# Performance work log

Hardware: AMD Instinct MI355X
Metric: run time of the kernel (lower is better)

Reference implementation:

```python
import jax, jax.numpy as jnp
import numpy as np

# AWQ packing: nibble for unpacked column j (within a packed int32 of 8 values)
# lives at bit offset 4 * AWQ_ORDER[j]  (the 'reverse AWQ order').
AWQ_ORDER = (0, 4, 1, 5, 2, 6, 3, 7)
GROUP_SIZE = 128


def _unpack_int4(packed):
    """[R, C] int32 -> [R, 8*C] int32 of 4-bit values in AWQ order."""
    shifts = jnp.array(AWQ_ORDER, dtype=jnp.int32) * 4  # [8]
    nib = jnp.right_shift(packed[:, :, None], shifts) & 0xF  # [R, C, 8]
    return nib.reshape(packed.shape[0], -1)


def setup_inputs() -> dict:
    key = jax.random.key(0)
    k1, k2, k3, k4 = jax.random.split(key, 4)
    M, K, N = 1024, 4096, 11008
    G = K // GROUP_SIZE  # 32
    x = jax.random.normal(k1, (M, K), dtype=jnp.float32)
    imin = jnp.iinfo(jnp.int32).min
    imax = jnp.iinfo(jnp.int32).max
    qweight = jax.random.randint(k2, (K, N // 8), imin, imax, dtype=jnp.int32)
    qzeros = jax.random.randint(k3, (G, N // 8), imin, imax, dtype=jnp.int32)
    scales = jax.random.uniform(k4, (G, N), dtype=jnp.float32, minval=0.001, maxval=0.01)
    return {"x": x, "qweight": qweight, "scales": scales, "qzeros": qzeros}


def reference(x, qweight, scales, qzeros):
    # Dequantize: W[k, n] = (w4[k, n] - z4[k//gs, n]) * scales[k//gs, n]
    K = qweight.shape[0]
    gs = K // qzeros.shape[0]  # group size
    w4 = _unpack_int4(qweight).astype(jnp.float32)   # [K, N]
    z4 = _unpack_int4(qzeros).astype(jnp.float32)    # [G, N]
    z = jnp.repeat(z4, gs, axis=0)                   # [K, N]
    s = jnp.repeat(scales, gs, axis=0)               # [K, N]
    W = (w4 - z) * s                                 # [K, N]
    # FP16_MATMUL_HEURISTIC path: dequantize then plain matmul
    return jnp.matmul(x, W)                          # [M, N]
```

## Files before the change

### kernel.cpp

```cpp
#include <hip/hip_runtime.h>
#include <stdint.h>

#define M_DIM 1024
#define K_DIM 4096
#define N_DIM 11008
#define NC_DIM 1376
#define G_DIM 32
#define GS 128

typedef __bf16 bf16x8 __attribute__((ext_vector_type(8)));
typedef float f32x4 __attribute__((ext_vector_type(4)));
typedef unsigned short ushort8 __attribute__((ext_vector_type(8)));

typedef __attribute__((address_space(1))) char as1_char;
typedef __attribute__((address_space(3))) char as3_char;
#define GLDS16(g, l) __builtin_amdgcn_global_load_lds((as1_char*)(g), (as3_char*)(l), 16, 0, 0)

static __device__ __forceinline__ int awq_shift(int j) {
  return ((j & 1) << 4) | ((j >> 1) << 2);
}

static __device__ __forceinline__ unsigned short f2bf(float f) {
  union { float f; uint32_t u; } c; c.f = f;
  uint32_t u = c.u;
  return (unsigned short)((u + 0x7FFFu + ((u >> 16) & 1u)) >> 16);
}

__global__ void k_cvt_x(const float* __restrict__ x, unsigned short* __restrict__ xb) {
  int i = blockIdx.x * blockDim.x + threadIdx.x;
  int base = i * 8;
  float4 v0 = *(const float4*)(x + base);
  float4 v1 = *(const float4*)(x + base + 4);
  ushort8 o;
  o[0] = f2bf(v0.x); o[1] = f2bf(v0.y); o[2] = f2bf(v0.z); o[3] = f2bf(v0.w);
  o[4] = f2bf(v1.x); o[5] = f2bf(v1.y); o[6] = f2bf(v1.z); o[7] = f2bf(v1.w);
  *(ushort8*)(xb + base) = o;
}

__global__ void k_dequant(const int* __restrict__ qw, const float* __restrict__ scales,
                          const int* __restrict__ qz, unsigned short* __restrict__ wt) {
  __shared__ int wlds[64][17];
  const int t = threadIdx.x;
  const int k0 = blockIdx.x * 64;
  const int nb = blockIdx.y;
  const int n_glob0 = nb * 128;
  const int c0 = n_glob0 >> 3;
  const int g = k0 >> 7;
#pragma unroll
  for (int p = 0; p < 4; ++p) {
    int idx = p * 256 + t;
    int k = idx >> 4, c = idx & 15;
    wlds[k][c] = qw[(size_t)(k0 + k) * NC_DIM + c0 + c];
  }
  __syncthreads();
#pragma unroll
  for (int p = 0; p < 4; ++p) {
    int u = p * 256 + t;
    int k8 = u & 7;
    int nl = u >> 3;
    int j = nl & 7;
    int c = nl >> 3;
    int shift = awq_shift(j);
    float s = scales[(size_t)g * N_DIM + n_glob0 + nl];
    int zw = qz[(size_t)g * NC_DIM + c0 + c];
    float zs = (float)((zw >> shift) & 0xF) * s;
    ushort8 o;
#pragma unroll
    for (int i = 0; i < 8; ++i) {
      int wv = wlds[k8 * 8 + i][c];
      int nib = (wv >> shift) & 0xF;
      o[i] = f2bf(fmaf((float)nib, s, -zs));
    }
    *(ushort8*)(wt + (size_t)(nb * 128 + nl) * K_DIM + k0 + k8 * 8) = o;
  }
}

#define BK 64
#define NT (K_DIM / BK)
#define REG_BYTES 16384

__device__ __forceinline__ void stage_half(const unsigned short* __restrict__ src, int row0, int T,
                                           unsigned char* lds_region, int w, int lane) {
  const int kb = (((lane & 7) ^ ((lane >> 3) & 7)) << 4);
  const int row = w * 16 + (lane >> 3);
  const unsigned short* g = src + (size_t)(row0 + row) * K_DIM + T * 64 + (kb >> 1);
  unsigned char* l = lds_region + w * 2048;
  GLDS16(g, l);
  GLDS16(g + (size_t)8 * K_DIM, l + 1024);
}

#define RD(base, off) (*(const bf16x8*)((const unsigned char*)(base) + (off)))
#define MFMA16(a, b, c) __builtin_amdgcn_mfma_f32_16x16x32_bf16((a), (b), (c), 0, 0, 0)

__launch_bounds__(512, 2)
__global__ void k_gemm8(const unsigned short* __restrict__ A,
                        const unsigned short* __restrict__ Bt,
                        float* __restrict__ C) {
  __shared__ __attribute__((aligned(16))) unsigned char LDS[131072];

  const int tid = threadIdx.x;
  const int lane = tid & 63;
  const int w = tid >> 6;
  const int wm = w >> 2;
  const int wn = w & 3;
  const int u = lane & 15;
  const int h = lane >> 4;
  const int xor16 = (lane & 7) << 4;
  const int kpos0 = (h * 16) ^ xor16;
  const int kpos1 = (64 + h * 16) ^ xor16;
  const int aoff = u * 128;

  const int orig = blockIdx.x;
  const int xcd = orig & 7, loc = orig >> 3;
  const int qq = 21, rr = 4;
  const int swz = (xcd < rr) ? xcd * (qq + 1) + loc : rr * (qq + 1) + (xcd - rr) * qq + loc;
  const int m0 = (swz & 3) * 256;
  const int nb0 = (swz >> 2) * 256;

  f32x4 acc[8][4] = {};

  stage_half(A,  m0,        0, LDS + 0 * REG_BYTES, w, lane);
  stage_half(A,  m0 + 128,  0, LDS + 1 * REG_BYTES, w, lane);
  stage_half(Bt, nb0,       0, LDS + 2 * REG_BYTES, w, lane);
  stage_half(Bt, nb0 + 128, 0, LDS + 3 * REG_BYTES, w, lane);
  stage_half(Bt, nb0,       1, LDS + 65536 + 2 * REG_BYTES, w, lane);
  stage_half(A,  m0,        1, LDS + 65536 + 0 * REG_BYTES, w, lane);
  asm volatile("s_waitcnt vmcnt(4)" ::: "memory");
  __builtin_amdgcn_s_barrier();

#pragma unroll 2
  for (int t = 0; t < NT; ++t) {
    const int cur = t & 1;
    unsigned char* bufc = LDS + cur * 65536;
    unsigned char* bufn = LDS + (cur ^ 1) * 65536;
    const unsigned char* rA = bufc + wm * REG_BYTES;
    const unsigned char* rB = bufc + (2 + (wn >> 1)) * REG_BYTES;
    const int bsub = (wn & 1) * 8192;

    bf16x8 aR[4][2], bLo[2][2], bHi[2][2];

#pragma unroll
    for (int mi = 0; mi < 4; ++mi) {
      aR[mi][0] = RD(rA, mi * 2048 + aoff + kpos0);
      aR[mi][1] = RD(rA, mi * 2048 + aoff + kpos1);
    }
#pragma unroll
    for (int nf = 0; nf < 2; ++nf) {
      bLo[nf][0] = RD(rB, bsub + nf * 2048 + aoff + kpos0);
      bLo[nf][1] = RD(rB, bsub + nf * 2048 + aoff + kpos1);
    }
    if (t + 1 < NT) stage_half(A, m0 + 128, t + 1, bufn + 1 * REG_BYTES, w, lane);
    __builtin_amdgcn_s_barrier();
    __builtin_amdgcn_s_setprio(1);
#pragma unroll
    for (int mi = 0; mi < 4; ++mi)
#pragma unroll
      for (int nf = 0; nf < 2; ++nf) {
        acc[mi][nf] = MFMA16(aR[mi][0], bLo[nf][0], acc[mi][nf]);
        acc[mi][nf] = MFMA16(aR[mi][1], bLo[nf][1], acc[mi][nf]);
      }
    __builtin_amdgcn_s_setprio(0);
    __builtin_amdgcn_s_barrier();

#pragma unroll
    for (int nf = 0; nf < 2; ++nf) {
      bHi[nf][0] = RD(rB, bsub + (nf + 2) * 2048 + aoff + kpos0);
      bHi[nf][1] = RD(rB, bsub + (nf + 2) * 2048 + aoff + kpos1);
    }
    if (t + 1 < NT) stage_half(Bt, nb0 + 128, t + 1, bufn + 3 * REG_BYTES, w, lane);
    __builtin_amdgcn_s_barrier();
    __builtin_amdgcn_s_setprio(1);
#pragma unroll
    for (int mi = 0; mi < 4; ++mi)
#pragma unroll
      for (int nf = 0; nf < 2; ++nf) {
        acc[mi][nf + 2] = MFMA16(aR[mi][0], bHi[nf][0], acc[mi][nf + 2]);
        acc[mi][nf + 2] = MFMA16(aR[mi][1], bHi[nf][1], acc[mi][nf + 2]);
      }
    __builtin_amdgcn_s_setprio(0);
    __builtin_amdgcn_s_barrier();

#pragma unroll
    for (int mi = 0; mi < 4; ++mi) {
      aR[mi][0] = RD(rA, (mi + 4) * 2048 + aoff + kpos0);
      aR[mi][1] = RD(rA, (mi + 4) * 2048 + aoff + kpos1);
    }
    if (t + 2 < NT) stage_half(Bt, nb0, t + 2, bufc + 2 * REG_BYTES, w, lane);
    __builtin_amdgcn_s_barrier();
    __builtin_amdgcn_s_setprio(1);
#pragma unroll
    for (int mi = 0; mi < 4; ++mi)
#pragma unroll
      for (int nf = 0; nf < 2; ++nf) {
        acc[mi + 4][nf + 2] = MFMA16(aR[mi][0], bHi[nf][0], acc[mi + 4][nf + 2]);
        acc[mi + 4][nf + 2] = MFMA16(aR[mi][1], bHi[nf][1], acc[mi + 4][nf + 2]);
      }
    __builtin_amdgcn_s_setprio(0);
    __builtin_amdgcn_s_barrier();

    if (t + 2 < NT) stage_half(A, m0, t + 2, bufc + 0 * REG_BYTES, w, lane);
    __builtin_amdgcn_s_barrier();
    __builtin_amdgcn_s_setprio(1);
#pragma unroll
    for (int mi = 0; mi < 4; ++mi)
#pragma unroll
      for (int nf = 0; nf < 2; ++nf) {
        acc[mi + 4][nf] = MFMA16(aR[mi][0], bLo[nf][0], acc[mi + 4][nf]);
        acc[mi + 4][nf] = MFMA16(aR[mi][1], bLo[nf][1], acc[mi + 4][nf]);
      }
    __builtin_amdgcn_s_setprio(0);
    if (t < NT - 2) {
      asm volatile("s_waitcnt vmcnt(4)" ::: "memory");
    } else {
      asm volatile("s_waitcnt vmcnt(0)" ::: "memory");
    }
    __builtin_amdgcn_s_barrier();
  }

  const int crow0 = m0 + wm * 128 + h * 4;
  const int ccol0 = nb0 + wn * 64 + u;
#pragma unroll
  for (int mi = 0; mi < 8; ++mi)
#pragma unroll
    for (int nf = 0; nf < 4; ++nf)
#pragma unroll
      for (int r = 0; r < 4; ++r)
        C[(size_t)(crow0 + mi * 16 + r) * N_DIM + ccol0 + nf * 16] = acc[mi][nf][r];
}

__global__ void k_fallback(const float* __restrict__ x, const int* __restrict__ qw,
                           const float* __restrict__ scales, const int* __restrict__ qz,
                           float* __restrict__ C) {
  int t = blockIdx.x * 256 + threadIdx.x;
  int m = t / NC_DIM;
  int c = t % NC_DIM;
  float acc[8];
#pragma unroll
  for (int j = 0; j < 8; ++j) acc[j] = 0.f;
  for (int g = 0; g < G_DIM; ++g) {
    int zw = qz[(size_t)g * NC_DIM + c];
    float sj[8], zsj[8];
#pragma unroll
    for (int j = 0; j < 8; ++j) {
      sj[j] = scales[(size_t)g * N_DIM + c * 8 + j];
      zsj[j] = (float)((zw >> awq_shift(j)) & 0xF) * sj[j];
    }
    for (int k = g * GS; k < (g + 1) * GS; ++k) {
      float xv = x[(size_t)m * K_DIM + k];
      int wv = qw[(size_t)k * NC_DIM + c];
#pragma unroll
      for (int j = 0; j < 8; ++j) {
        float dq = fmaf((float)((wv >> awq_shift(j)) & 0xF), sj[j], -zsj[j]);
        acc[j] = fmaf(xv, dq, acc[j]);
      }
    }
  }
#pragma unroll
  for (int j = 0; j < 8; ++j)
    C[(size_t)m * N_DIM + c * 8 + j] = acc[j];
}

extern "C" void kernel_launch(void* const* d_in, const int* in_sizes, int n_in,
                              void* d_out, int out_size, void* d_ws, size_t ws_size,
                              hipStream_t stream) {
  (void)in_sizes; (void)n_in; (void)out_size;
  const float* x = (const float*)d_in[0];
  const int* qw = (const int*)d_in[1];
  const float* scales = (const float*)d_in[2];
  const int* qz = (const int*)d_in[3];
  float* C = (float*)d_out;

  const size_t xb_bytes = (size_t)M_DIM * K_DIM * 2;
  const size_t wt_bytes = (size_t)N_DIM * K_DIM * 2;

  if (ws_size >= xb_bytes + wt_bytes) {
    unsigned short* xb = (unsigned short*)d_ws;
    unsigned short* wt = (unsigned short*)((char*)d_ws + xb_bytes);
    k_cvt_x<<<(M_DIM * K_DIM) / (256 * 8), 256, 0, stream>>>(x, xb);
    dim3 gd(K_DIM / 64, N_DIM / 128);
    k_dequant<<<gd, 256, 0, stream>>>(qw, scales, qz, wt);
    k_gemm8<<<(M_DIM / 256) * (N_DIM / 256), 512, 0, stream>>>(xb, wt, C);
  } else {
    k_fallback<<<(M_DIM * NC_DIM) / 256, 256, 0, stream>>>(x, qw, scales, qz, C);
  }
}
```

Baseline: 131.3 us.

## Switch GEMM inner loop to 32x32x16 bf16 MFMA with reshaped fragments

Replaces the 16x16x32 MFMA tiling with 32x32x16 bf16 MFMA, so each wave holds 4x2 32x32 accumulators instead of 8x4 16x16 ones. LDS fragment reads, the swizzled k positions and the output store mapping are reworked to match. The global-to-LDS staging helper is turned into a macro with precomputed base pointers to cut per-iteration address arithmetic. The larger MFMA needs fewer LDS reads per flop, at the cost of different register pressure and a more scattered output store pattern.

```diff
diff --git a/kernel.cpp b/kernel.cpp
--- a/kernel.cpp
+++ b/kernel.cpp
@@ -9,7 +9,7 @@
 #define GS 128
 
 typedef __bf16 bf16x8 __attribute__((ext_vector_type(8)));
-typedef float f32x4 __attribute__((ext_vector_type(4)));
+typedef float f32x16 __attribute__((ext_vector_type(16)));
 typedef unsigned short ushort8 __attribute__((ext_vector_type(8)));
 
 typedef __attribute__((address_space(1))) char as1_char;
@@ -79,18 +79,8 @@
 #define NT (K_DIM / BK)
 #define REG_BYTES 16384
 
-__device__ __forceinline__ void stage_half(const unsigned short* __restrict__ src, int row0, int T,
-                                           unsigned char* lds_region, int w, int lane) {
-  const int kb = (((lane & 7) ^ ((lane >> 3) & 7)) << 4);
-  const int row = w * 16 + (lane >> 3);
-  const unsigned short* g = src + (size_t)(row0 + row) * K_DIM + T * 64 + (kb >> 1);
-  unsigned char* l = lds_region + w * 2048;
-  GLDS16(g, l);
-  GLDS16(g + (size_t)8 * K_DIM, l + 1024);
-}
-
 #define RD(base, off) (*(const bf16x8*)((const unsigned char*)(base) + (off)))
-#define MFMA16(a, b, c) __builtin_amdgcn_mfma_f32_16x16x32_bf16((a), (b), (c), 0, 0, 0)
+#define MFMA32(a, b, c) __builtin_amdgcn_mfma_f32_32x32x16_bf16((a), (b), (c), 0, 0, 0)
 
 __launch_bounds__(512, 2)
 __global__ void k_gemm8(const unsigned short* __restrict__ A,
@@ -103,12 +93,13 @@
   const int w = tid >> 6;
   const int wm = w >> 2;
   const int wn = w & 3;
-  const int u = lane & 15;
-  const int h = lane >> 4;
-  const int xor16 = (lane & 7) << 4;
-  const int kpos0 = (h * 16) ^ xor16;
-  const int kpos1 = (64 + h * 16) ^ xor16;
-  const int aoff = u * 128;
+  const int r32 = lane & 31;
+  const int hh = lane >> 5;
+
+  const int xorr = (lane & 7) << 4;
+  int kpos[4];
+#pragma unroll
+  for (int ks = 0; ks < 4; ++ks) kpos[ks] = ((ks << 5) | (hh << 4)) ^ xorr;
 
   const int orig = blockIdx.x;
   const int xcd = orig & 7, loc = orig >> 3;
@@ -117,97 +108,96 @@
   const int m0 = (swz & 3) * 256;
   const int nb0 = (swz >> 2) * 256;
 
-  f32x4 acc[8][4] = {};
-
-  stage_half(A,  m0,        0, LDS + 0 * REG_BYTES, w, lane);
-  stage_half(A,  m0 + 128,  0, LDS + 1 * REG_BYTES, w, lane);
-  stage_half(Bt, nb0,       0, LDS + 2 * REG_BYTES, w, lane);
-  stage_half(Bt, nb0 + 128, 0, LDS + 3 * REG_BYTES, w, lane);
-  stage_half(Bt, nb0,       1, LDS + 65536 + 2 * REG_BYTES, w, lane);
-  stage_half(A,  m0,        1, LDS + 65536 + 0 * REG_BYTES, w, lane);
+  const int kb_src = (((lane & 7) ^ ((lane >> 3) & 7)) << 4) >> 1;
+  const int srow = w * 16 + (lane >> 3);
+  const unsigned short* gA0 = A + (size_t)(m0 + srow) * K_DIM + kb_src;
+  const unsigned short* gA1 = gA0 + (size_t)128 * K_DIM;
+  const unsigned short* gB0 = Bt + (size_t)(nb0 + srow) * K_DIM + kb_src;
+  const unsigned short* gB1 = gB0 + (size_t)128 * K_DIM;
+  const int ldsw = w * 2048;
+
+#define STAGE(gp, T, bufoff, region)                                              \
+  do {                                                                            \
+    const unsigned short* _g = (gp) + (size_t)(T) * 64;                           \
+    unsigned char* _l = LDS + (bufoff) + (region) * REG_BYTES + ldsw;             \
+    GLDS16(_g, _l);                                                               \
+    GLDS16(_g + (size_t)8 * K_DIM, _l + 1024);                                    \
+  } while (0)
+
+  f32x16 acc[4][2] = {};
+
+  STAGE(gA0, 0, 0, 0);
+  STAGE(gA1, 0, 0, 1);
+  STAGE(gB0, 0, 0, 2);
+  STAGE(gB1, 0, 0, 3);
+  STAGE(gB0, 1, 65536, 2);
+  STAGE(gA0, 1, 65536, 0);
   asm volatile("s_waitcnt vmcnt(4)" ::: "memory");
   __builtin_amdgcn_s_barrier();
 
 #pragma unroll 2
   for (int t = 0; t < NT; ++t) {
     const int cur = t & 1;
-    unsigned char* bufc = LDS + cur * 65536;
-    unsigned char* bufn = LDS + (cur ^ 1) * 65536;
-    const unsigned char* rA = bufc + wm * REG_BYTES;
-    const unsigned char* rB = bufc + (2 + (wn >> 1)) * REG_BYTES;
-    const int bsub = (wn & 1) * 8192;
-
-    bf16x8 aR[4][2], bLo[2][2], bHi[2][2];
-
-#pragma unroll
-    for (int mi = 0; mi < 4; ++mi) {
-      aR[mi][0] = RD(rA, mi * 2048 + aoff + kpos0);
-      aR[mi][1] = RD(rA, mi * 2048 + aoff + kpos1);
-    }
-#pragma unroll
-    for (int nf = 0; nf < 2; ++nf) {
-      bLo[nf][0] = RD(rB, bsub + nf * 2048 + aoff + kpos0);
-      bLo[nf][1] = RD(rB, bsub + nf * 2048 + aoff + kpos1);
-    }
-    if (t + 1 < NT) stage_half(A, m0 + 128, t + 1, bufn + 1 * REG_BYTES, w, lane);
-    __builtin_amdgcn_s_barrier();
-    __builtin_amdgcn_s_setprio(1);
-#pragma unroll
-    for (int mi = 0; mi < 4; ++mi)
-#pragma unroll
-      for (int nf = 0; nf < 2; ++nf) {
-        acc[mi][nf] = MFMA16(aR[mi][0], bLo[nf][0], acc[mi][nf]);
-        acc[mi][nf] = MFMA16(aR[mi][1], bLo[nf][1], acc[mi][nf]);
-      }
-    __builtin_amdgcn_s_setprio(0);
-    __builtin_amdgcn_s_barrier();
-
-#pragma unroll
-    for (int nf = 0; nf < 2; ++nf) {
-      bHi[nf][0] = RD(rB, bsub + (nf + 2) * 2048 + aoff + kpos0);
-      bHi[nf][1] = RD(rB, bsub + (nf + 2) * 2048 + aoff + kpos1);
-    }
-    if (t + 1 < NT) stage_half(Bt, nb0 + 128, t + 1, bufn + 3 * REG_BYTES, w, lane);
-    __builtin_amdgcn_s_barrier();
-    __builtin_amdgcn_s_setprio(1);
-#pragma unroll
-    for (int mi = 0; mi < 4; ++mi)
-#pragma unroll
-      for (int nf = 0; nf < 2; ++nf) {
-        acc[mi][nf + 2] = MFMA16(aR[mi][0], bHi[nf][0], acc[mi][nf + 2]);
-        acc[mi][nf + 2] = MFMA16(aR[mi][1], bHi[nf][1], acc[mi][nf + 2]);
-      }
-    __builtin_amdgcn_s_setprio(0);
-    __builtin_amdgcn_s_barrier();
-
-#pragma unroll
-    for (int mi = 0; mi < 4; ++mi) {
-      aR[mi][0] = RD(rA, (mi + 4) * 2048 + aoff + kpos0);
-      aR[mi][1] = RD(rA, (mi + 4) * 2048 + aoff + kpos1);
-    }
-    if (t + 2 < NT) stage_half(Bt, nb0, t + 2, bufc + 2 * REG_BYTES, w, lane);
-    __builtin_amdgcn_s_barrier();
-    __builtin_amdgcn_s_setprio(1);
-#pragma unroll
-    for (int mi = 0; mi < 4; ++mi)
-#pragma unroll
-      for (int nf = 0; nf < 2; ++nf) {
-        acc[mi + 4][nf + 2] = MFMA16(aR[mi][0], bHi[nf][0], acc[mi + 4][nf + 2]);
-        acc[mi + 4][nf + 2] = MFMA16(aR[mi][1], bHi[nf][1], acc[mi + 4][nf + 2]);
-      }
-    __builtin_amdgcn_s_setprio(0);
-    __builtin_amdgcn_s_barrier();
-
-    if (t + 2 < NT) stage_half(A, m0, t + 2, bufc + 0 * REG_BYTES, w, lane);
-    __builtin_amdgcn_s_barrier();
-    __builtin_amdgcn_s_setprio(1);
-#pragma unroll
-    for (int mi = 0; mi < 4; ++mi)
-#pragma unroll
-      for (int nf = 0; nf < 2; ++nf) {
-        acc[mi + 4][nf] = MFMA16(aR[mi][0], bLo[nf][0], acc[mi + 4][nf]);
-        acc[mi + 4][nf] = MFMA16(aR[mi][1], bLo[nf][1], acc[mi + 4][nf]);
-      }
+    const int bo_c = cur * 65536;
+    const int bo_n = (cur ^ 1) * 65536;
+    const unsigned char* rdA = LDS + bo_c + wm * REG_BYTES + r32 * 128;
+    const unsigned char* rdB = LDS + bo_c + (2 + (wn >> 1)) * REG_BYTES + (wn & 1) * 8192 + r32 * 128;
+
+    bf16x8 aF[2][4], bA[4], bB[4];
+
+#pragma unroll
+    for (int ks = 0; ks < 4; ++ks) bA[ks] = RD(rdB, kpos[ks]);
+#pragma unroll
+    for (int rb = 0; rb < 2; ++rb)
+#pragma unroll
+      for (int ks = 0; ks < 4; ++ks) aF[rb][ks] = RD(rdA, rb * 4096 + kpos[ks]);
+    if (t + 1 < NT) STAGE(gA1, t + 1, bo_n, 1);
+    __builtin_amdgcn_s_barrier();
+    __builtin_amdgcn_s_setprio(1);
+#pragma unroll
+    for (int ks = 0; ks < 4; ++ks) {
+      acc[0][0] = MFMA32(aF[0][ks], bA[ks], acc[0][0]);
+      acc[1][0] = MFMA32(aF[1][ks], bA[ks], acc[1][0]);
+    }
+    __builtin_amdgcn_s_setprio(0);
+    __builtin_amdgcn_s_barrier();
+
+#pragma unroll
+    for (int ks = 0; ks < 4; ++ks) bB[ks] = RD(rdB, 4096 + kpos[ks]);
+    if (t + 1 < NT) STAGE(gB1, t + 1, bo_n, 3);
+    __builtin_amdgcn_s_barrier();
+    __builtin_amdgcn_s_setprio(1);
+#pragma unroll
+    for (int ks = 0; ks < 4; ++ks) {
+      acc[0][1] = MFMA32(aF[0][ks], bB[ks], acc[0][1]);
+      acc[1][1] = MFMA32(aF[1][ks], bB[ks], acc[1][1]);
+    }
+    __builtin_amdgcn_s_setprio(0);
+    __builtin_amdgcn_s_barrier();
+
+#pragma unroll
+    for (int rb = 0; rb < 2; ++rb)
+#pragma unroll
+      for (int ks = 0; ks < 4; ++ks) aF[rb][ks] = RD(rdA, (rb + 2) * 4096 + kpos[ks]);
+    if (t + 2 < NT) STAGE(gB0, t + 2, bo_c, 2);
+    __builtin_amdgcn_s_barrier();
+    __builtin_amdgcn_s_setprio(1);
+#pragma unroll
+    for (int ks = 0; ks < 4; ++ks) {
+      acc[2][1] = MFMA32(aF[0][ks], bB[ks], acc[2][1]);
+      acc[3][1] = MFMA32(aF[1][ks], bB[ks], acc[3][1]);
+    }
+    __builtin_amdgcn_s_setprio(0);
+    __builtin_amdgcn_s_barrier();
+
+    if (t + 2 < NT) STAGE(gA0, t + 2, bo_c, 0);
+    __builtin_amdgcn_s_barrier();
+    __builtin_amdgcn_s_setprio(1);
+#pragma unroll
+    for (int ks = 0; ks < 4; ++ks) {
+      acc[2][0] = MFMA32(aF[0][ks], bA[ks], acc[2][0]);
+      acc[3][0] = MFMA32(aF[1][ks], bA[ks], acc[3][0]);
+    }
     __builtin_amdgcn_s_setprio(0);
     if (t < NT - 2) {
       asm volatile("s_waitcnt vmcnt(4)" ::: "memory");
@@ -217,15 +207,19 @@
     __builtin_amdgcn_s_barrier();
   }
 
-  const int crow0 = m0 + wm * 128 + h * 4;
-  const int ccol0 = nb0 + wn * 64 + u;
-#pragma unroll
-  for (int mi = 0; mi < 8; ++mi)
-#pragma unroll
-    for (int nf = 0; nf < 4; ++nf)
-#pragma unroll
-      for (int r = 0; r < 4; ++r)
-        C[(size_t)(crow0 + mi * 16 + r) * N_DIM + ccol0 + nf * 16] = acc[mi][nf][r];
+  const int ccol = nb0 + wn * 64 + r32;
+  const int crow_base = m0 + wm * 128 + 4 * hh;
+#pragma unroll
+  for (int rb = 0; rb < 4; ++rb)
+#pragma unroll
+    for (int cb = 0; cb < 2; ++cb) {
+      f32x16 v = acc[rb][cb];
+#pragma unroll
+      for (int reg = 0; reg < 16; ++reg) {
+        int row = crow_base + rb * 32 + (reg & 3) + 8 * (reg >> 2);
+        C[(size_t)row * N_DIM + ccol + cb * 32] = v[reg];
+      }
+    }
 }
 
 __global__ void k_fallback(const float* __restrict__ x, const int* __restrict__ qw,
```

After: 135.1 us. 1.03x slower.

## Fuse int4 dequantization into GEMM mainloop using repacked weights and scale tables

Applied to the files above, without the earlier changes.

Replaces the separate bf16 weight dequantization pass with a repack kernel that transposes int4 nibbles into K-packed words, plus a small table of per-group scale and zero*scale. The GEMM now stages the packed int4 words into LDS and dequantizes them in registers to bf16 right before the MFMAs. This cuts the weight traffic into the GEMM and removes the write and read of a full bf16 weight matrix. In exchange it adds VALU work in the mainloop, and it keeps an unused k_gemm8 variant alongside the launched k_gemm8_fixed.

```diff
diff --git a/kernel.cpp b/kernel.cpp
--- a/kernel.cpp
+++ b/kernel.cpp
@@ -10,6 +10,7 @@
 
 typedef __bf16 bf16x8 __attribute__((ext_vector_type(8)));
 typedef float f32x4 __attribute__((ext_vector_type(4)));
+typedef float f32x2 __attribute__((ext_vector_type(2)));
 typedef unsigned short ushort8 __attribute__((ext_vector_type(8)));
 
 typedef __attribute__((address_space(1))) char as1_char;
@@ -37,66 +38,50 @@
   *(ushort8*)(xb + base) = o;
 }
 
-__global__ void k_dequant(const int* __restrict__ qw, const float* __restrict__ scales,
-                          const int* __restrict__ qz, unsigned short* __restrict__ wt) {
-  __shared__ int wlds[64][17];
-  const int t = threadIdx.x;
-  const int k0 = blockIdx.x * 64;
-  const int nb = blockIdx.y;
-  const int n_glob0 = nb * 128;
-  const int c0 = n_glob0 >> 3;
-  const int g = k0 >> 7;
-#pragma unroll
-  for (int p = 0; p < 4; ++p) {
-    int idx = p * 256 + t;
-    int k = idx >> 4, c = idx & 15;
-    wlds[k][c] = qw[(size_t)(k0 + k) * NC_DIM + c0 + c];
+__global__ void k_wqt(const int* __restrict__ qw, int* __restrict__ Wq) {
+  int t = blockIdx.x * 256 + threadIdx.x;
+  int wr = t / NC_DIM, c = t % NC_DIM;
+  int in[8];
+#pragma unroll
+  for (int j = 0; j < 8; ++j) in[j] = qw[(size_t)(wr * 8 + j) * NC_DIM + c];
+  int out[8];
+#pragma unroll
+  for (int j2 = 0; j2 < 8; ++j2) {
+    int sh = awq_shift(j2);
+    int o = 0;
+#pragma unroll
+    for (int j = 0; j < 8; ++j) o |= ((in[j] >> sh) & 0xF) << (4 * j);
+    out[j2] = o;
   }
-  __syncthreads();
-#pragma unroll
-  for (int p = 0; p < 4; ++p) {
-    int u = p * 256 + t;
-    int k8 = u & 7;
-    int nl = u >> 3;
-    int j = nl & 7;
-    int c = nl >> 3;
-    int shift = awq_shift(j);
-    float s = scales[(size_t)g * N_DIM + n_glob0 + nl];
-    int zw = qz[(size_t)g * NC_DIM + c0 + c];
-    float zs = (float)((zw >> shift) & 0xF) * s;
-    ushort8 o;
-#pragma unroll
-    for (int i = 0; i < 8; ++i) {
-      int wv = wlds[k8 * 8 + i][c];
-      int nib = (wv >> shift) & 0xF;
-      o[i] = f2bf(fmaf((float)nib, s, -zs));
-    }
-    *(ushort8*)(wt + (size_t)(nb * 128 + nl) * K_DIM + k0 + k8 * 8) = o;
-  }
-}
-
-#define BK 64
-#define NT (K_DIM / BK)
+  int4* dst = (int4*)(Wq + (size_t)wr * N_DIM + c * 8);
+  dst[0] = make_int4(out[0], out[1], out[2], out[3]);
+  dst[1] = make_int4(out[4], out[5], out[6], out[7]);
+}
+
+__global__ void k_tab(const int* __restrict__ qz, const float* __restrict__ scales,
+                      float* __restrict__ SZ) {
+  int t = blockIdx.x * 256 + threadIdx.x;
+  int g = t / N_DIM, n = t % N_DIM;
+  float s = scales[t];
+  int z = (qz[(size_t)g * NC_DIM + (n >> 3)] >> awq_shift(n & 7)) & 0xF;
+  f32x2 v; v[0] = s; v[1] = (float)z * s;
+  *(f32x2*)(SZ + (size_t)t * 2) = v;
+}
+
+#define NT (K_DIM / 64)
 #define REG_BYTES 16384
-
-__device__ __forceinline__ void stage_half(const unsigned short* __restrict__ src, int row0, int T,
-                                           unsigned char* lds_region, int w, int lane) {
-  const int kb = (((lane & 7) ^ ((lane >> 3) & 7)) << 4);
-  const int row = w * 16 + (lane >> 3);
-  const unsigned short* g = src + (size_t)(row0 + row) * K_DIM + T * 64 + (kb >> 1);
-  unsigned char* l = lds_region + w * 2048;
-  GLDS16(g, l);
-  GLDS16(g + (size_t)8 * K_DIM, l + 1024);
-}
+#define BW_OFF 65536
 
 #define RD(base, off) (*(const bf16x8*)((const unsigned char*)(base) + (off)))
 #define MFMA16(a, b, c) __builtin_amdgcn_mfma_f32_16x16x32_bf16((a), (b), (c), 0, 0, 0)
+#define SBAR0() __builtin_amdgcn_sched_barrier(0)
 
 __launch_bounds__(512, 2)
 __global__ void k_gemm8(const unsigned short* __restrict__ A,
-                        const unsigned short* __restrict__ Bt,
+                        const int* __restrict__ Wq,
+                        const float* __restrict__ SZ,
                         float* __restrict__ C) {
-  __shared__ __attribute__((aligned(16))) unsigned char LDS[131072];
+  __shared__ __attribute__((aligned(16))) unsigned char LDS[73792];
 
   const int tid = threadIdx.x;
   const int lane = tid & 63;
@@ -104,10 +89,10 @@
   const int wm = w >> 2;
   const int wn = w & 3;
   const int u = lane & 15;
-  const int h = lane >> 4;
+  const int h4 = lane >> 4;
   const int xor16 = (lane & 7) << 4;
-  const int kpos0 = (h * 16) ^ xor16;
-  const int kpos1 = (64 + h * 16) ^ xor16;
+  const int kpos0 = (h4 * 16) ^ xor16;
+  const int kpos1 = (64 + h4 * 16) ^ xor16;
   const int aoff = u * 128;
 
   const int orig = blockIdx.x;
@@ -117,107 +102,321 @@
   const int m0 = (swz & 3) * 256;
   const int nb0 = (swz >> 2) * 256;
 
+  const int kb_src = (((lane & 7) ^ ((lane >> 3) & 7)) << 4) >> 1;
+  const int srow = w * 16 + (lane >> 3);
+  const unsigned short* gA0 = A + (size_t)(m0 + srow) * K_DIM + kb_src;
+  const unsigned short* gA1 = gA0 + (size_t)128 * K_DIM;
+  const int ldsw = w * 2048;
+
+#define STAGE_A(gp, T, bufoff, region)                                            \
+  do {                                                                            \
+    const unsigned short* _g = (gp) + (size_t)(T) * 64;                           \
+    unsigned char* _l = LDS + (bufoff) + (region) * REG_BYTES + ldsw;             \
+    GLDS16(_g, _l);                                                               \
+    GLDS16(_g + (size_t)8 * K_DIM, _l + 1024);                                    \
+  } while (0)
+
+  const int* gBw = Wq + (size_t)w * N_DIM + nb0 + lane * 4;
+#define STAGE_BW(T) GLDS16(gBw + (size_t)(T) * 8 * N_DIM, LDS + BW_OFF + w * 1032)
+
+  const int n_base = nb0 + wn * 64 + u;
+  const unsigned char* rdBw = LDS + BW_OFF + h4 * 1032 + (wn * 64 + u) * 4;
+
   f32x4 acc[8][4] = {};
-
-  stage_half(A,  m0,        0, LDS + 0 * REG_BYTES, w, lane);
-  stage_half(A,  m0 + 128,  0, LDS + 1 * REG_BYTES, w, lane);
-  stage_half(Bt, nb0,       0, LDS + 2 * REG_BYTES, w, lane);
-  stage_half(Bt, nb0 + 128, 0, LDS + 3 * REG_BYTES, w, lane);
-  stage_half(Bt, nb0,       1, LDS + 65536 + 2 * REG_BYTES, w, lane);
-  stage_half(A,  m0,        1, LDS + 65536 + 0 * REG_BYTES, w, lane);
-  asm volatile("s_waitcnt vmcnt(4)" ::: "memory");
+  f32x2 sz[4];
+
+  STAGE_A(gA0, 0, 0, 0);
+  STAGE_A(gA1, 0, 0, 1);
+  STAGE_BW(0);
+  SBAR0();
+#pragma unroll
+  for (int nf = 0; nf < 4; ++nf)
+    sz[nf] = *(const f32x2*)(SZ + ((size_t)0 * N_DIM + n_base + nf * 16) * 2);
+  SBAR0();
+  STAGE_A(gA0, 1, 65536 - 65536 + 65536, 0);
+  asm volatile("s_waitcnt vmcnt(2)" ::: "memory");
   __builtin_amdgcn_s_barrier();
 
 #pragma unroll 2
   for (int t = 0; t < NT; ++t) {
     const int cur = t & 1;
-    unsigned char* bufc = LDS + cur * 65536;
-    unsigned char* bufn = LDS + (cur ^ 1) * 65536;
-    const unsigned char* rA = bufc + wm * REG_BYTES;
-    const unsigned char* rB = bufc + (2 + (wn >> 1)) * REG_BYTES;
-    const int bsub = (wn & 1) * 8192;
-
-    bf16x8 aR[4][2], bLo[2][2], bHi[2][2];
-
+    const int bo_c = cur * 32768;
+    const int bo_n = (cur ^ 1) * 32768;
+    const unsigned char* rdA = LDS + bo_c + wm * REG_BYTES;
+
+    bf16x8 aR[4][2], bF[4][2];
+    int wrd[4][2];
+
+#pragma unroll
+    for (int nf = 0; nf < 4; ++nf)
+#pragma unroll
+      for (int ks = 0; ks < 2; ++ks)
+        wrd[nf][ks] = *(const int*)(rdBw + ks * 4128 + nf * 64);
 #pragma unroll
     for (int mi = 0; mi < 4; ++mi) {
-      aR[mi][0] = RD(rA, mi * 2048 + aoff + kpos0);
-      aR[mi][1] = RD(rA, mi * 2048 + aoff + kpos1);
-    }
-#pragma unroll
-    for (int nf = 0; nf < 2; ++nf) {
-      bLo[nf][0] = RD(rB, bsub + nf * 2048 + aoff + kpos0);
-      bLo[nf][1] = RD(rB, bsub + nf * 2048 + aoff + kpos1);
-    }
-    if (t + 1 < NT) stage_half(A, m0 + 128, t + 1, bufn + 1 * REG_BYTES, w, lane);
-    __builtin_amdgcn_s_barrier();
-    __builtin_amdgcn_s_setprio(1);
-#pragma unroll
-    for (int mi = 0; mi < 4; ++mi)
-#pragma unroll
-      for (int nf = 0; nf < 2; ++nf) {
-        acc[mi][nf] = MFMA16(aR[mi][0], bLo[nf][0], acc[mi][nf]);
-        acc[mi][nf] = MFMA16(aR[mi][1], bLo[nf][1], acc[mi][nf]);
-      }
-    __builtin_amdgcn_s_setprio(0);
-    __builtin_amdgcn_s_barrier();
-
-#pragma unroll
-    for (int nf = 0; nf < 2; ++nf) {
-      bHi[nf][0] = RD(rB, bsub + (nf + 2) * 2048 + aoff + kpos0);
-      bHi[nf][1] = RD(rB, bsub + (nf + 2) * 2048 + aoff + kpos1);
-    }
-    if (t + 1 < NT) stage_half(Bt, nb0 + 128, t + 1, bufn + 3 * REG_BYTES, w, lane);
-    __builtin_amdgcn_s_barrier();
-    __builtin_amdgcn_s_setprio(1);
-#pragma unroll
-    for (int mi = 0; mi < 4; ++mi)
-#pragma unroll
-      for (int nf = 0; nf < 2; ++nf) {
-        acc[mi][nf + 2] = MFMA16(aR[mi][0], bHi[nf][0], acc[mi][nf + 2]);
-        acc[mi][nf + 2] = MFMA16(aR[mi][1], bHi[nf][1], acc[mi][nf + 2]);
+      aR[mi][0] = RD(rdA, mi * 2048 + aoff + kpos0);
+      aR[mi][1] = RD(rdA, mi * 2048 + aoff + kpos1);
+    }
+    if (t + 1 < NT) STAGE_A(gA1, t + 1, bo_n, 1);
+#pragma unroll
+    for (int nf = 0; nf < 2; ++nf)
+#pragma unroll
+      for (int ks = 0; ks < 2; ++ks) {
+        int wv = wrd[nf][ks];
+        float s = sz[nf][0], zz = sz[nf][1];
+        bf16x8 f;
+#pragma unroll
+        for (int j = 0; j < 8; ++j)
+          f[j] = (__bf16)fmaf((float)((wv >> (4 * j)) & 0xF), s, -zz);
+        bF[nf][ks] = f;
+      }
+    __builtin_amdgcn_s_barrier();
+    __builtin_amdgcn_s_setprio(1);
+#pragma unroll
+    for (int mi = 0; mi < 4; ++mi)
+#pragma unroll
+      for (int nf = 0; nf < 2; ++nf) {
+        acc[mi][nf] = MFMA16(aR[mi][0], bF[nf][0], acc[mi][nf]);
+        acc[mi][nf] = MFMA16(aR[mi][1], bF[nf][1], acc[mi][nf]);
+      }
+    __builtin_amdgcn_s_setprio(0);
+    __builtin_amdgcn_s_barrier();
+
+    if (t + 1 < NT) STAGE_BW(t + 1);
+    SBAR0();
+    if ((t & 1) && (t + 1 < NT)) {
+      const int gg = (t + 1) >> 1;
+#pragma unroll
+      for (int nf = 0; nf < 4; ++nf)
+        sz[nf] = *(const f32x2*)(SZ + ((size_t)gg * N_DIM + n_base + nf * 16) * 2);
+    }
+    SBAR0();
+#pragma unroll
+    for (int nf = 2; nf < 4; ++nf)
+#pragma unroll
+      for (int ks = 0; ks < 2; ++ks) {
+        int wv = wrd[nf][ks];
+        float s = sz[nf][0], zz = sz[nf][1];
+        bf16x8 f;
+#pragma unroll
+        for (int j = 0; j < 8; ++j)
+          f[j] = (__bf16)fmaf((float)((wv >> (4 * j)) & 0xF), s, -zz);
+        bF[nf][ks] = f;
+      }
+    __builtin_amdgcn_s_barrier();
+    __builtin_amdgcn_s_setprio(1);
+#pragma unroll
+    for (int mi = 0; mi < 4; ++mi)
+#pragma unroll
+      for (int nf = 0; nf < 2; ++nf) {
+        acc[mi][nf + 2] = MFMA16(aR[mi][0], bF[nf + 2][0], acc[mi][nf + 2]);
+        acc[mi][nf + 2] = MFMA16(aR[mi][1], bF[nf + 2][1], acc[mi][nf + 2]);
       }
     __builtin_amdgcn_s_setprio(0);
     __builtin_amdgcn_s_barrier();
 
 #pragma unroll
     for (int mi = 0; mi < 4; ++mi) {
-      aR[mi][0] = RD(rA, (mi + 4) * 2048 + aoff + kpos0);
-      aR[mi][1] = RD(rA, (mi + 4) * 2048 + aoff + kpos1);
-    }
-    if (t + 2 < NT) stage_half(Bt, nb0, t + 2, bufc + 2 * REG_BYTES, w, lane);
-    __builtin_amdgcn_s_barrier();
-    __builtin_amdgcn_s_setprio(1);
-#pragma unroll
-    for (int mi = 0; mi < 4; ++mi)
-#pragma unroll
-      for (int nf = 0; nf < 2; ++nf) {
-        acc[mi + 4][nf + 2] = MFMA16(aR[mi][0], bHi[nf][0], acc[mi + 4][nf + 2]);
-        acc[mi + 4][nf + 2] = MFMA16(aR[mi][1], bHi[nf][1], acc[mi + 4][nf + 2]);
-      }
-    __builtin_amdgcn_s_setprio(0);
-    __builtin_amdgcn_s_barrier();
-
-    if (t + 2 < NT) stage_half(A, m0, t + 2, bufc + 0 * REG_BYTES, w, lane);
-    __builtin_amdgcn_s_barrier();
-    __builtin_amdgcn_s_setprio(1);
-#pragma unroll
-    for (int mi = 0; mi < 4; ++mi)
-#pragma unroll
-      for (int nf = 0; nf < 2; ++nf) {
-        acc[mi + 4][nf] = MFMA16(aR[mi][0], bLo[nf][0], acc[mi + 4][nf]);
-        acc[mi + 4][nf] = MFMA16(aR[mi][1], bLo[nf][1], acc[mi + 4][nf]);
+      aR[mi][0] = RD(rdA, (mi + 4) * 2048 + aoff + kpos0);
+      aR[mi][1] = RD(rdA, (mi + 4) * 2048 + aoff + kpos1);
+    }
+    __builtin_amdgcn_s_barrier();
+    __builtin_amdgcn_s_setprio(1);
+#pragma unroll
+    for (int mi = 0; mi < 4; ++mi)
+#pragma unroll
+      for (int nf = 0; nf < 2; ++nf) {
+        acc[mi + 4][nf + 2] = MFMA16(aR[mi][0], bF[nf + 2][0], acc[mi + 4][nf + 2]);
+        acc[mi + 4][nf + 2] = MFMA16(aR[mi][1], bF[nf + 2][1], acc[mi + 4][nf + 2]);
+      }
+    __builtin_amdgcn_s_setprio(0);
+    __builtin_amdgcn_s_barrier();
+
+    if (t + 2 < NT) STAGE_A(gA0, t + 2, bo_c, 0);
+    __builtin_amdgcn_s_barrier();
+    __builtin_amdgcn_s_setprio(1);
+#pragma unroll
+    for (int mi = 0; mi < 4; ++mi)
+#pragma unroll
+      for (int nf = 0; nf < 2; ++nf) {
+        acc[mi + 4][nf] = MFMA16(aR[mi][0], bF[nf][0], acc[mi + 4][nf]);
+        acc[mi + 4][nf] = MFMA16(aR[mi][1], bF[nf][1], acc[mi + 4][nf]);
       }
     __builtin_amdgcn_s_setprio(0);
     if (t < NT - 2) {
-      asm volatile("s_waitcnt vmcnt(4)" ::: "memory");
+      asm volatile("s_waitcnt vmcnt(2)" ::: "memory");
     } else {
       asm volatile("s_waitcnt vmcnt(0)" ::: "memory");
     }
     __builtin_amdgcn_s_barrier();
   }
 
-  const int crow0 = m0 + wm * 128 + h * 4;
+  const int crow0 = m0 + wm * 128 + h4 * 4;
+  const int ccol0 = nb0 + wn * 64 + u;
+#pragma unroll
+  for (int mi = 0; mi < 8; ++mi)
+#pragma unroll
+    for (int nf = 0; nf < 4; ++nf)
+#pragma unroll
+      for (int r = 0; r < 4; ++r)
+        C[(size_t)(crow0 + mi * 16 + r) * N_DIM + ccol0 + nf * 16] = acc[mi][nf][r];
+}
+
+
+__launch_bounds__(512, 2)
+__global__ void k_gemm8_fixed(const unsigned short* __restrict__ A,
+                              const int* __restrict__ Wq,
+                              const float* __restrict__ SZ,
+                              float* __restrict__ C) {
+  __shared__ __attribute__((aligned(16))) unsigned char LDS[73792];
+
+  const int tid = threadIdx.x;
+  const int lane = tid & 63;
+  const int w = tid >> 6;
+  const int wm = w >> 2;
+  const int wn = w & 3;
+  const int u = lane & 15;
+  const int h4 = lane >> 4;
+  const int xor16 = (lane & 7) << 4;
+  const int kpos0 = (h4 * 16) ^ xor16;
+  const int kpos1 = (64 + h4 * 16) ^ xor16;
+  const int aoff = u * 128;
+
+  const int orig = blockIdx.x;
+  const int xcd = orig & 7, loc = orig >> 3;
+  const int qq = 21, rr = 4;
+  const int swz = (xcd < rr) ? xcd * (qq + 1) + loc : rr * (qq + 1) + (xcd - rr) * qq + loc;
+  const int m0 = (swz & 3) * 256;
+  const int nb0 = (swz >> 2) * 256;
+
+  const int kb_src = (((lane & 7) ^ ((lane >> 3) & 7)) << 4) >> 1;
+  const int srow = w * 16 + (lane >> 3);
+  const unsigned short* gA0 = A + (size_t)(m0 + srow) * K_DIM + kb_src;
+  const unsigned short* gA1 = gA0 + (size_t)128 * K_DIM;
+  const int ldsw = w * 2048;
+
+  const int* gBw = Wq + (size_t)w * N_DIM + nb0 + lane * 4;
+  const int n_base = nb0 + wn * 64 + u;
+  const unsigned char* rdBw = LDS + BW_OFF + h4 * 1032 + (wn * 64 + u) * 4;
+
+  f32x4 acc[8][4] = {};
+  f32x2 sz[4];
+
+  STAGE_A(gA0, 0, 0, 0);
+  STAGE_A(gA1, 0, 0, 1);
+  STAGE_BW(0);
+  SBAR0();
+#pragma unroll
+  for (int nf = 0; nf < 4; ++nf)
+    sz[nf] = *(const f32x2*)(SZ + ((size_t)(n_base + nf * 16)) * 2);
+  SBAR0();
+  STAGE_A(gA0, 1, 32768, 0);
+  asm volatile("s_waitcnt vmcnt(2)" ::: "memory");
+  __builtin_amdgcn_s_barrier();
+
+#pragma unroll 2
+  for (int t = 0; t < NT; ++t) {
+    const int cur = t & 1;
+    const int bo_c = cur * 32768;
+    const int bo_n = (cur ^ 1) * 32768;
+    const unsigned char* rdA = LDS + bo_c + wm * REG_BYTES;
+
+    bf16x8 aR[4][2], bF[4][2];
+    int wrd[4][2];
+
+#pragma unroll
+    for (int nf = 0; nf < 4; ++nf)
+#pragma unroll
+      for (int ks = 0; ks < 2; ++ks)
+        wrd[nf][ks] = *(const int*)(rdBw + ks * 4128 + nf * 64);
+#pragma unroll
+    for (int mi = 0; mi < 4; ++mi) {
+      aR[mi][0] = RD(rdA, mi * 2048 + aoff + kpos0);
+      aR[mi][1] = RD(rdA, mi * 2048 + aoff + kpos1);
+    }
+    if (t + 1 < NT) STAGE_A(gA1, t + 1, bo_n, 1);
+#pragma unroll
+    for (int nf = 0; nf < 4; ++nf)
+#pragma unroll
+      for (int ks = 0; ks < 2; ++ks) {
+        int wv = wrd[nf][ks];
+        float s = sz[nf][0], zz = sz[nf][1];
+        bf16x8 f;
+#pragma unroll
+        for (int j = 0; j < 8; ++j)
+          f[j] = (__bf16)fmaf((float)((wv >> (4 * j)) & 0xF), s, -zz);
+        bF[nf][ks] = f;
+      }
+    __builtin_amdgcn_s_barrier();
+    __builtin_amdgcn_s_setprio(1);
+#pragma unroll
+    for (int mi = 0; mi < 4; ++mi)
+#pragma unroll
+      for (int nf = 0; nf < 2; ++nf) {
+        acc[mi][nf] = MFMA16(aR[mi][0], bF[nf][0], acc[mi][nf]);
+        acc[mi][nf] = MFMA16(aR[mi][1], bF[nf][1], acc[mi][nf]);
+      }
+    __builtin_amdgcn_s_setprio(0);
+    __builtin_amdgcn_s_barrier();
+
+    if (t + 1 < NT) STAGE_BW(t + 1);
+    SBAR0();
+    if ((t & 1) && (t + 1 < NT)) {
+      const int gg = (t + 1) >> 1;
+#pragma unroll
+      for (int nf = 0; nf < 4; ++nf)
+        sz[nf] = *(const f32x2*)(SZ + ((size_t)gg * N_DIM + n_base + nf * 16) * 2);
+    }
+    SBAR0();
+    __builtin_amdgcn_s_barrier();
+    __builtin_amdgcn_s_setprio(1);
+#pragma unroll
+    for (int mi = 0; mi < 4; ++mi)
+#pragma unroll
+      for (int nf = 0; nf < 2; ++nf) {
+        acc[mi][nf + 2] = MFMA16(aR[mi][0], bF[nf + 2][0], acc[mi][nf + 2]);
+        acc[mi][nf + 2] = MFMA16(aR[mi][1], bF[nf + 2][1], acc[mi][nf + 2]);
+      }
+    __builtin_amdgcn_s_setprio(0);
+    __builtin_amdgcn_s_barrier();
+
+#pragma unroll
+    for (int mi = 0; mi < 4; ++mi) {
+      aR[mi][0] = RD(rdA, (mi + 4) * 2048 + aoff + kpos0);
+      aR[mi][1] = RD(rdA, (mi + 4) * 2048 + aoff + kpos1);
+    }
+    __builtin_amdgcn_s_barrier();
+    __builtin_amdgcn_s_setprio(1);
+#pragma unroll
+    for (int mi = 0; mi < 4; ++mi)
+#pragma unroll
+      for (int nf = 0; nf < 2; ++nf) {
+        acc[mi + 4][nf + 2] = MFMA16(aR[mi][0], bF[nf + 2][0], acc[mi + 4][nf + 2]);
+        acc[mi + 4][nf + 2] = MFMA16(aR[mi][1], bF[nf + 2][1], acc[mi + 4][nf + 2]);
+      }
+    __builtin_amdgcn_s_setprio(0);
+    __builtin_amdgcn_s_barrier();
+
+    if (t + 2 < NT) STAGE_A(gA0, t + 2, bo_c, 0);
+    __builtin_amdgcn_s_barrier();
+    __builtin_amdgcn_s_setprio(1);
+#pragma unroll
+    for (int mi = 0; mi < 4; ++mi)
+#pragma unroll
+      for (int nf = 0; nf < 2; ++nf) {
+        acc[mi + 4][nf] = MFMA16(aR[mi][0], bF[nf][0], acc[mi + 4][nf]);
+        acc[mi + 4][nf] = MFMA16(aR[mi][1], bF[nf][1], acc[mi + 4][nf]);
+      }
+    __builtin_amdgcn_s_setprio(0);
+    if (t < NT - 2) {
+      asm volatile("s_waitcnt vmcnt(2)" ::: "memory");
+    } else {
+      asm volatile("s_waitcnt vmcnt(0)" ::: "memory");
+    }
+    __builtin_amdgcn_s_barrier();
+  }
+
+  const int crow0 = m0 + wm * 128 + h4 * 4;
   const int ccol0 = nb0 + wn * 64 + u;
 #pragma unroll
   for (int mi = 0; mi < 8; ++mi)
@@ -271,15 +470,17 @@
   float* C = (float*)d_out;
 
   const size_t xb_bytes = (size_t)M_DIM * K_DIM * 2;
-  const size_t wt_bytes = (size_t)N_DIM * K_DIM * 2;
-
-  if (ws_size >= xb_bytes + wt_bytes) {
+  const size_t wq_bytes = (size_t)(K_DIM / 8) * N_DIM * 4;
+  const size_t sz_bytes = (size_t)G_DIM * N_DIM * 2 * 4;
+
+  if (ws_size >= xb_bytes + wq_bytes + sz_bytes) {
     unsigned short* xb = (unsigned short*)d_ws;
-    unsigned short* wt = (unsigned short*)((char*)d_ws + xb_bytes);
+    int* Wq = (int*)((char*)d_ws + xb_bytes);
+    float* SZ = (float*)((char*)d_ws + xb_bytes + wq_bytes);
     k_cvt_x<<<(M_DIM * K_DIM) / (256 * 8), 256, 0, stream>>>(x, xb);
-    dim3 gd(K_DIM / 64, N_DIM / 128);
-    k_dequant<<<gd, 256, 0, stream>>>(qw, scales, qz, wt);
-    k_gemm8<<<(M_DIM / 256) * (N_DIM / 256), 512, 0, stream>>>(xb, wt, C);
+    k_wqt<<<(K_DIM / 8) * NC_DIM / 256, 256, 0, stream>>>(qw, Wq);
+    k_tab<<<G_DIM * N_DIM / 256, 256, 0, stream>>>(qz, scales, SZ);
+    k_gemm8_fixed<<<(M_DIM / 256) * (N_DIM / 256), 512, 0, stream>>>(xb, Wq, SZ, C);
   } else {
     k_fallback<<<(M_DIM * NC_DIM) / 256, 256, 0, stream>>>(x, qw, scales, qz, C);
   }
```

After: 180.3 us. 37.3% more time.
